# Kernel optimization log

Hardware: AMD Instinct MI355X
Metric: run time of the kernel (lower is better)

## Reference

```python
import jax, jax.numpy as jnp
import numpy as np

WEIGHT = 1e-7       # lambda for the CRF loss
SIGMA_RGB = 15.0    # color-similarity bandwidth
SIGMA_XY = 100.0    # spatial-proximity bandwidth
SCALE = 0.5         # scale_factor (sigma_xy is multiplied by it in forward)


def setup_inputs() -> dict:
    key = jax.random.key(0)
    k1, k2 = jax.random.split(key)
    images = jax.random.uniform(k1, (4, 3, 128, 128), jnp.float32) * 255.0  # [0,255] RGB
    logits = jax.random.normal(k2, (4, 4, 128, 128), jnp.float32)
    segmentations = jax.nn.softmax(logits, axis=1)  # softmaxed logits, N*K*H*W
    return {"images": images, "segmentations": segmentations}


def _crf_loss(images, segmentations):
    n, k, h, w = segmentations.shape
    # F.interpolate(images, scale_factor=0.5, mode='nearest') == stride-2 subsample
    img_s = images[:, :, ::2, ::2]
    # F.interpolate(segs, scale_factor=0.5, mode='bilinear', align_corners=False)
    # for exact /2 downscale == 2x2 average pooling
    hs, ws = h // 2, w // 2
    seg_s = segmentations.reshape(n, k, hs, 2, ws, 2).mean(axis=(3, 5))  # [n,k,hs,ws]

    P = hs * ws
    yy, xx = jnp.meshgrid(jnp.arange(hs, dtype=jnp.float32),
                          jnp.arange(ws, dtype=jnp.float32), indexing='ij')
    sigma_xy_eff = SIGMA_XY * SCALE
    pos = jnp.stack([xx, yy], axis=-1).reshape(P, 2) / sigma_xy_eff      # [P,2]
    rgb = img_s.reshape(n, 3, P).transpose(0, 2, 1) / SIGMA_RGB          # [n,P,3]
    feats = jnp.concatenate([jnp.broadcast_to(pos[None], (n, P, 2)), rgb], axis=-1)  # [n,P,5]

    # exact dense Gaussian bilateral kernel W_ij = exp(-0.5*||f_i - f_j||^2)
    sq = jnp.sum(feats * feats, axis=-1)                                 # [n,P]
    d2 = sq[:, :, None] + sq[:, None, :] - 2.0 * jnp.einsum('npc,nqc->npq', feats, feats)
    Wk = jnp.exp(-0.5 * jnp.maximum(d2, 0.0))                            # [n,P,P]

    S = seg_s.reshape(n, k, P)
    AS = jnp.einsum('npq,nkq->nkp', Wk, S)                               # bilateral-filtered segs
    loss = -jnp.sum(S * AS) / jnp.float32(n)
    return (WEIGHT * loss).reshape(1)


def reference(images, segmentations):
    return _crf_loss(images, segmentations)
```

## Files before the change

kernel.cpp:

```cpp
#include <hip/hip_runtime.h>

#define NB   4
#define KCH  4
#define PPB  4096
#define QT   64
#define BLK  256
#define PT   4
#define NBLK 160

#if __has_builtin(__builtin_amdgcn_exp2f)
#define EXPFN(x) __builtin_amdgcn_exp2f(x)
#define FSCALE 1.2011224087864498f
#else
#define EXPFN(x) __expf(x)
#define FSCALE 1.0f
#endif


__global__ __launch_bounds__(256) void crf_prep(const float* __restrict__ images,
                                                const float* __restrict__ segs,
                                                float4* __restrict__ RA,
                                                float4* __restrict__ RB,
                                                float2* __restrict__ RC,
                                                float* __restrict__ out) {
    int gid = blockIdx.x * BLK + threadIdx.x;
    if (gid == 0) out[0] = 0.0f;
    int n = gid >> 12;
    int p = gid & (PPB - 1);
    int i = p >> 6;
    int j = p & 63;
    int off = 256 * i + 2 * j;
    const float* img = images + (size_t)n * 3 * 16384;
    float x = (float)j * (FSCALE / 50.0f);
    float y = (float)i * (FSCALE / 50.0f);
    float r = img[off]         * (FSCALE / 15.0f);
    float g = img[16384 + off] * (FSCALE / 15.0f);
    float b = img[32768 + off] * (FSCALE / 15.0f);
    float h = -0.5f * (x * x + y * y + r * r + g * g + b * b);
    const float* sg = segs + (size_t)n * KCH * 16384;
    float s0, s1, s2, s3;
    {
        float2 u0 = *(const float2*)(sg + off);
        float2 u1 = *(const float2*)(sg + off + 128);
        s0 = 0.25f * ((u0.x + u0.y) + (u1.x + u1.y));
        u0 = *(const float2*)(sg + 16384 + off);
        u1 = *(const float2*)(sg + 16384 + off + 128);
        s1 = 0.25f * ((u0.x + u0.y) + (u1.x + u1.y));
        u0 = *(const float2*)(sg + 32768 + off);
        u1 = *(const float2*)(sg + 32768 + off + 128);
        s2 = 0.25f * ((u0.x + u0.y) + (u1.x + u1.y));
        u0 = *(const float2*)(sg + 49152 + off);
        u1 = *(const float2*)(sg + 49152 + off + 128);
        s3 = 0.25f * ((u0.x + u0.y) + (u1.x + u1.y));
    }
    RA[gid] = make_float4(x, y, r, g);
    RB[gid] = make_float4(b, h, s0, s1);
    RC[gid] = make_float2(s2, s3);
}

__global__ __launch_bounds__(256) void crf_pairs(const float4* __restrict__ RA,
                                                 const float4* __restrict__ RB,
                                                 const float2* __restrict__ RC,
                                                 float* __restrict__ out) {
    __shared__ float4 ldsA[QT + 1];
    __shared__ float4 ldsB[QT + 1];
    __shared__ float2 ldsC[QT + 1];
    __shared__ float wsum[BLK / 64];

    int t = threadIdx.x;
    int n = blockIdx.y;

    int b = blockIdx.x;
    int pt = (b >= 64) + (b >= 112) + (b >= 144);
    int qc = b - 8 * pt * (7 - pt);
    int pbase = pt * (BLK * PT);
    int qbase = qc * QT;
    bool mixed = (qc >> 4) == pt;
    int base = n << 12;

    if (t < QT)            ldsA[t]          = RA[base + qbase + t];
    else if (t < 2 * QT)   ldsB[t - QT]     = RB[base + qbase + (t - QT)];
    else if (t < 3 * QT)   ldsC[t - 2 * QT] = RC[base + qbase + (t - 2 * QT)];

    float4 pa[PT], pb[PT];
    float2 pc[PT];
#pragma unroll
    for (int pi = 0; pi < PT; ++pi) {
        int idx = base + pbase + t + pi * BLK;
        pa[pi] = RA[idx];
        pb[pi] = RB[idx];
        pc[pi] = RC[idx];
    }
    __syncthreads();

    float acc[PT] = {0.f, 0.f, 0.f, 0.f};
    float acc_all;

    float4 fa = ldsA[0];
    float4 fb = ldsB[0];
    float2 fc = ldsC[0];

    if (!mixed) {
#pragma unroll 2
        for (int q = 0; q < QT; ++q) {
            float4 na = ldsA[q + 1];
            float4 nb = ldsB[q + 1];
            float2 nc = ldsC[q + 1];
#pragma unroll
            for (int pi = 0; pi < PT; ++pi) {
                float d = pb[pi].y + fb.y;
                d = fmaf(pa[pi].x, fa.x, d);
                d = fmaf(pa[pi].y, fa.y, d);
                d = fmaf(pa[pi].z, fa.z, d);
                d = fmaf(pa[pi].w, fa.w, d);
                d = fmaf(pb[pi].x, fb.x, d);
                float w = EXPFN(d);
                float sd = pb[pi].z * fb.z;
                sd = fmaf(pb[pi].w, fb.w, sd);
                sd = fmaf(pc[pi].x, fc.x, sd);
                sd = fmaf(pc[pi].y, fc.y, sd);
                acc[pi] = fmaf(w, sd, acc[pi]);
            }
            fa = na; fb = nb; fc = nc;
        }
        acc_all = 2.0f * ((acc[0] + acc[1]) + (acc[2] + acc[3]));
    } else {
#pragma unroll 2
        for (int q = 0; q < QT; ++q) {
            float4 na = ldsA[q + 1];
            float4 nb = ldsB[q + 1];
            float2 nc = ldsC[q + 1];
            int qg = qbase + q;
#pragma unroll
            for (int pi = 0; pi < PT; ++pi) {
                int pg = pbase + t + pi * BLK;
                float d = pb[pi].y + fb.y;
                d = fmaf(pa[pi].x, fa.x, d);
                d = fmaf(pa[pi].y, fa.y, d);
                d = fmaf(pa[pi].z, fa.z, d);
                d = fmaf(pa[pi].w, fa.w, d);
                d = fmaf(pb[pi].x, fb.x, d);
                float w = EXPFN(d);
                float sd = pb[pi].z * fb.z;
                sd = fmaf(pb[pi].w, fb.w, sd);
                sd = fmaf(pc[pi].x, fc.x, sd);
                sd = fmaf(pc[pi].y, fc.y, sd);
                float f = (qg > pg) ? 2.0f : ((qg == pg) ? 1.0f : 0.0f);
                acc[pi] = fmaf(w, sd * f, acc[pi]);
            }
            fa = na; fb = nb; fc = nc;
        }
        acc_all = (acc[0] + acc[1]) + (acc[2] + acc[3]);
    }

#pragma unroll
    for (int off = 32; off > 0; off >>= 1)
        acc_all += __shfl_down(acc_all, off, 64);
    if ((t & 63) == 0) wsum[t >> 6] = acc_all;
    __syncthreads();
    if (t == 0) {
        float s = (wsum[0] + wsum[1]) + (wsum[2] + wsum[3]);
        atomicAdd(out, s * (-2.5e-8f));
    }
}

extern "C" void kernel_launch(void* const* d_in, const int* in_sizes, int n_in,
                              void* d_out, int out_size, void* d_ws, size_t ws_size,
                              hipStream_t stream) {
    const float* images = (const float*)d_in[0];
    const float* segs   = (const float*)d_in[1];
    float* out = (float*)d_out;
    char* ws = (char*)d_ws;
    float4* RA = (float4*)(ws);
    float4* RB = (float4*)(ws + 262144);
    float2* RC = (float2*)(ws + 524288);
    (void)in_sizes; (void)n_in; (void)out_size; (void)ws_size;

    crf_prep<<<dim3(64), dim3(256), 0, stream>>>(images, segs, RA, RB, RC, out);
    crf_pairs<<<dim3(NBLK, NB), dim3(256), 0, stream>>>(RA, RB, RC, out);
}
```

Measured before the change: 77.78 us.

## Shrink p-tile to one point per thread and launch more triangular blocks

Each thread now handles one p point per block instead of four, and the triangular block enumeration is remapped to 16 p-tiles of 256 points, giving 544 blocks per image instead of 160. The goal is more parallelism and better load balance across the GPU's compute units for this small problem, plus a smaller register footprint. In exchange, each block redoes the LDS q-tile load for four times less compute, the per-block reduction and atomic count grow, and the diagonal masked blocks become a larger share of the work.

After: 91.17 us. +17.2%, slower.

```diff
diff --git a/kernel.cpp b/kernel.cpp
--- a/kernel.cpp
+++ b/kernel.cpp
@@ -5,8 +5,7 @@
 #define PPB  4096
 #define QT   64
 #define BLK  256
-#define PT   4
-#define NBLK 160
+#define NBLK 544
 
 #if __has_builtin(__builtin_amdgcn_exp2f)
 #define EXPFN(x) __builtin_amdgcn_exp2f(x)
@@ -71,29 +70,25 @@
     int n = blockIdx.y;
 
     int b = blockIdx.x;
-    int pt = (b >= 64) + (b >= 112) + (b >= 144);
-    int qc = b - 8 * pt * (7 - pt);
-    int pbase = pt * (BLK * PT);
+    int pc = 0;
+#pragma unroll
+    for (int i = 1; i < 16; ++i) pc += (b >= 2 * i * (33 - i)) ? 1 : 0;
+    int qc = b - 2 * pc * (33 - pc) + 4 * pc;
+    int pbase = pc * BLK;
     int qbase = qc * QT;
-    bool mixed = (qc >> 4) == pt;
+    bool mixed = (qc >> 2) == pc;
     int base = n << 12;
 
     if (t < QT)            ldsA[t]          = RA[base + qbase + t];
     else if (t < 2 * QT)   ldsB[t - QT]     = RB[base + qbase + (t - QT)];
     else if (t < 3 * QT)   ldsC[t - 2 * QT] = RC[base + qbase + (t - 2 * QT)];
 
-    float4 pa[PT], pb[PT];
-    float2 pc[PT];
-#pragma unroll
-    for (int pi = 0; pi < PT; ++pi) {
-        int idx = base + pbase + t + pi * BLK;
-        pa[pi] = RA[idx];
-        pb[pi] = RB[idx];
-        pc[pi] = RC[idx];
-    }
+    float4 pa = RA[base + pbase + t];
+    float4 pb = RB[base + pbase + t];
+    float2 pc2 = RC[base + pbase + t];
     __syncthreads();
 
-    float acc[PT] = {0.f, 0.f, 0.f, 0.f};
+    float acc = 0.f;
     float acc_all;
 
     float4 fa = ldsA[0];
@@ -101,56 +96,50 @@
     float2 fc = ldsC[0];
 
     if (!mixed) {
-#pragma unroll 2
+#pragma unroll 4
         for (int q = 0; q < QT; ++q) {
             float4 na = ldsA[q + 1];
             float4 nb = ldsB[q + 1];
             float2 nc = ldsC[q + 1];
-#pragma unroll
-            for (int pi = 0; pi < PT; ++pi) {
-                float d = pb[pi].y + fb.y;
-                d = fmaf(pa[pi].x, fa.x, d);
-                d = fmaf(pa[pi].y, fa.y, d);
-                d = fmaf(pa[pi].z, fa.z, d);
-                d = fmaf(pa[pi].w, fa.w, d);
-                d = fmaf(pb[pi].x, fb.x, d);
-                float w = EXPFN(d);
-                float sd = pb[pi].z * fb.z;
-                sd = fmaf(pb[pi].w, fb.w, sd);
-                sd = fmaf(pc[pi].x, fc.x, sd);
-                sd = fmaf(pc[pi].y, fc.y, sd);
-                acc[pi] = fmaf(w, sd, acc[pi]);
-            }
+            float d = pb.y + fb.y;
+            d = fmaf(pa.x, fa.x, d);
+            d = fmaf(pa.y, fa.y, d);
+            d = fmaf(pa.z, fa.z, d);
+            d = fmaf(pa.w, fa.w, d);
+            d = fmaf(pb.x, fb.x, d);
+            float w = EXPFN(d);
+            float sd = pb.z * fb.z;
+            sd = fmaf(pb.w, fb.w, sd);
+            sd = fmaf(pc2.x, fc.x, sd);
+            sd = fmaf(pc2.y, fc.y, sd);
+            acc = fmaf(w, sd, acc);
             fa = na; fb = nb; fc = nc;
         }
-        acc_all = 2.0f * ((acc[0] + acc[1]) + (acc[2] + acc[3]));
+        acc_all = 2.0f * acc;
     } else {
-#pragma unroll 2
+        int pg = pbase + t;
+#pragma unroll 4
         for (int q = 0; q < QT; ++q) {
             float4 na = ldsA[q + 1];
             float4 nb = ldsB[q + 1];
             float2 nc = ldsC[q + 1];
             int qg = qbase + q;
-#pragma unroll
-            for (int pi = 0; pi < PT; ++pi) {
-                int pg = pbase + t + pi * BLK;
-                float d = pb[pi].y + fb.y;
-                d = fmaf(pa[pi].x, fa.x, d);
-                d = fmaf(pa[pi].y, fa.y, d);
-                d = fmaf(pa[pi].z, fa.z, d);
-                d = fmaf(pa[pi].w, fa.w, d);
-                d = fmaf(pb[pi].x, fb.x, d);
-                float w = EXPFN(d);
-                float sd = pb[pi].z * fb.z;
-                sd = fmaf(pb[pi].w, fb.w, sd);
-                sd = fmaf(pc[pi].x, fc.x, sd);
-                sd = fmaf(pc[pi].y, fc.y, sd);
-                float f = (qg > pg) ? 2.0f : ((qg == pg) ? 1.0f : 0.0f);
-                acc[pi] = fmaf(w, sd * f, acc[pi]);
-            }
+            float d = pb.y + fb.y;
+            d = fmaf(pa.x, fa.x, d);
+            d = fmaf(pa.y, fa.y, d);
+            d = fmaf(pa.z, fa.z, d);
+            d = fmaf(pa.w, fa.w, d);
+            d = fmaf(pb.x, fb.x, d);
+            float w = EXPFN(d);
+            float sd = pb.z * fb.z;
+            sd = fmaf(pb.w, fb.w, sd);
+            sd = fmaf(pc2.x, fc.x, sd);
+            sd = fmaf(pc2.y, fc.y, sd);
+            float f = (qg > pg) ? 2.0f : ((qg == pg) ? 1.0f : 0.0f);
+            acc = fmaf(w, sd * f, acc);
             fa = na; fb = nb; fc = nc;
         }
-        acc_all = (acc[0] + acc[1]) + (acc[2] + acc[3]);
+        acc_all = acc;
     }
 
 #pragma unroll
```
